# Kernel tuning notes

Measured on AMD Instinct MI355X. Metric: run time of the kernel, lower is better.

Reference implementation:

```python
import jax, jax.numpy as jnp
import numpy as np

THRESH = 0.3   # vis_threshold (score filter and final keep threshold)
SIGMA = 0.5    # Gaussian soft-NMS sigma (method=2 in classic soft_nms)
B, N = 16, 2048


def setup_inputs() -> dict:
    key = jax.random.key(0)
    k1, k2, k3 = jax.random.split(key, 3)
    xy = jax.random.uniform(k1, (B, N, 2), dtype=jnp.float32) * 1024.0
    wh = jax.random.uniform(k2, (B, N, 2), dtype=jnp.float32) * 256.0 + 1.0
    scores = jax.random.uniform(k3, (B, N, 1), dtype=jnp.float32)
    detections = jnp.concatenate([xy, xy + wh, scores], axis=-1)  # [B,N,5]
    return {"detections": detections}


def _pairwise_iou(b):
    # b: [N,4] as (x1,y1,x2,y2); classic soft-NMS uses +1 area convention
    x1, y1, x2, y2 = b[:, 0], b[:, 1], b[:, 2], b[:, 3]
    area = (x2 - x1 + 1.0) * (y2 - y1 + 1.0)
    xx1 = jnp.maximum(x1[:, None], x1[None, :])
    yy1 = jnp.maximum(y1[:, None], y1[None, :])
    xx2 = jnp.minimum(x2[:, None], x2[None, :])
    yy2 = jnp.minimum(y2[:, None], y2[None, :])
    w = jnp.clip(xx2 - xx1 + 1.0, 0.0)
    h = jnp.clip(yy2 - yy1 + 1.0, 0.0)
    inter = w * h
    return inter / (area[:, None] + area[None, :] - inter)  # [N,N]


def _soft_nms_single(boxes, scores):
    # boxes: [N,4], scores: [N]
    n = scores.shape[0]
    iou = _pairwise_iou(boxes)            # [N,N]
    valid = scores > THRESH               # score-threshold prefilter
    s0 = jnp.where(valid, scores, 0.0)

    def step(carry, _):
        s, active = carry
        i = jnp.argmax(jnp.where(active, s, -1.0))     # greedy pick of max live score
        si = jnp.where(active[i], s[i], -1.0)          # -1 sentinel once all boxes consumed
        w = jnp.exp(-(iou[i] * iou[i]) / SIGMA)        # Gaussian decay (method=2)
        active = active.at[i].set(False)
        s = jnp.where(active, s * w, s)                # decay remaining live scores
        return (s, active), (i, si)

    _, (idx, picked) = jax.lax.scan(step, (s0, valid), None, length=n)
    # score each box carried at the moment it was picked; .max ignores -1 sentinels
    final = jnp.full((n,), -1.0, scores.dtype).at[idx].max(picked)
    keep = final > THRESH
    return final, keep


def reference(detections):
    boxes = detections[..., :4]   # [B,N,4]
    scores = detections[..., 4]   # [B,N]
    final, keep = jax.vmap(_soft_nms_single)(boxes, scores)
    return final, keep
```

## Files before the change

kernel.cpp:

```cpp
#include <hip/hip_runtime.h>
#include <stdint.h>

static constexpr float kThresh = 0.3f;
static constexpr int N    = 2048;
static constexpr int NT   = 256;
static constexpr int LPT  = N / NT;
static constexpr int NW   = NT / 64;
static constexpr int KMAX = 8;

using u64 = unsigned long long;
using u32 = unsigned int;

template <int CTRL>
__device__ __forceinline__ u64 dpp_max_u64_step(u64 k) {
    const int lo  = (int)(u32)k;
    const int hi  = (int)(u32)(k >> 32);
    const int mlo = __builtin_amdgcn_update_dpp(lo, lo, CTRL, 0xF, 0xF, false);
    const int mhi = __builtin_amdgcn_update_dpp(hi, hi, CTRL, 0xF, 0xF, false);
    const u64 m   = ((u64)(u32)mhi << 32) | (u32)mlo;
    return (m > k) ? m : k;
}
__device__ __forceinline__ u64 wave_max_u64(u64 k) {
    k = dpp_max_u64_step<0x111>(k);
    k = dpp_max_u64_step<0x112>(k);
    k = dpp_max_u64_step<0x114>(k);
    k = dpp_max_u64_step<0x118>(k);
    k = dpp_max_u64_step<0x142>(k);
    k = dpp_max_u64_step<0x143>(k);
    const int lo = __builtin_amdgcn_readlane((int)(u32)k, 63);
    const int hi = __builtin_amdgcn_readlane((int)(u32)(k >> 32), 63);
    return ((u64)(u32)hi << 32) | (u32)lo;
}

struct Pick {
    u32    mid;
    float4 box;
    float  area;
};

template <int K>
__device__ __forceinline__ u64 decay_and_keys(
        float (&sr)[KMAX], const float (&x1)[KMAX], const float (&y1)[KMAX],
        const float (&x2)[KMAX], const float (&y2)[KMAX], const float (&ar)[KMAX],
        const u32 (&jp)[KMAX], const Pick& w)
{
    u64 kmax = 0ULL;
    #pragma unroll
    for (int e = 0; e < K; ++e) {
        if (jp[e] == w.mid) sr[e] = -1.0f;
        const float xx1 = fmaxf(w.box.x, x1[e]);
        const float yy1 = fmaxf(w.box.y, y1[e]);
        const float xx2 = fminf(w.box.z, x2[e]);
        const float yy2 = fminf(w.box.w, y2[e]);
        const float ww  = fmaxf(xx2 - xx1 + 1.0f, 0.0f);
        const float hh  = fmaxf(yy2 - yy1 + 1.0f, 0.0f);
        const float inter = ww * hh;
        const float iou   = inter / (w.area + ar[e] - inter);
        sr[e] *= expf(-(iou * iou) * 2.0f);
        const u64 key = ((u64)(__float_as_uint(sr[e]) + 1u) << 32) | jp[e];
        const u64 kk  = (sr[e] >= 0.0f) ? key : 0ULL;
        if (kk > kmax) kmax = kk;
    }
    return kmax;
}

template <int K>
__device__ __forceinline__ void fill_slots(
        float (&sr)[KMAX], float (&x1)[KMAX], float (&y1)[KMAX],
        float (&x2)[KMAX], float (&y2)[KMAX], float (&ar)[KMAX], u32 (&jp)[KMAX],
        const int* slist, const float* srs, const float4* sbox, const float* sarea,
        int t, int alive)
{
    #pragma unroll
    for (int e = 0; e < K; ++e) {
        const int pos = t + NT * e;
        if (pos < alive) {
            const int j = slist[pos];
            sr[e] = srs[pos];
            const float4 bb = sbox[j];
            x1[e] = bb.x; y1[e] = bb.y; x2[e] = bb.z; y2[e] = bb.w;
            ar[e] = sarea[j];
            jp[e] = ((u32)(N - 1 - j) << 21) | ((u32)t << 13) | ((u32)e << 10);
        } else {
            sr[e] = -1.0f;
            x1[e] = 3.0e38f; y1[e] = 3.0e38f; x2[e] = -3.0e38f; y2[e] = -3.0e38f;
            ar[e] = 1.0f;
            jp[e] = 0x3FFu;
        }
    }
}

template <int K>
__device__ __forceinline__ void run_tier(
        int& alive, int& k, Pick& w,
        float (&sr)[KMAX], float (&x1)[KMAX], float (&y1)[KMAX],
        float (&x2)[KMAX], float (&y2)[KMAX], float (&ar)[KMAX], u32 (&jp)[KMAX],
        int* slist, float* srs, const float4* sbox, const float* sarea, float* sfin,
        u64 (*redk)[NW], int* swave, int t, int lane, int wid)
{
    const int floorA = (K > 1) ? NT * (K - 1) : 0;
    if (alive <= floorA) return;

    fill_slots<K>(sr, x1, y1, x2, y2, ar, jp, slist, srs, sbox, sarea, t, alive);

    const int passes = alive - floorA;
    for (int p = 0; p < passes; ++p) {
        const u64 kmax = decay_and_keys<K>(sr, x1, y1, x2, y2, ar, jp, w);
        const u64 wmax = wave_max_u64(kmax);
        const bool writer = (wmax != 0ULL) ? (kmax == wmax) : (lane == 0);
        if (writer) redk[k & 1][wid] = wmax;
        __syncthreads();
        u64 best = redk[k & 1][0];
        #pragma unroll
        for (int q = 1; q < NW; ++q) {
            const u64 o = redk[k & 1][q];
            if (o > best) best = o;
        }
        const u32 lo   = (u32)best;
        const int winJ = (N - 1) - (int)(lo >> 21);
        w.mid = lo & 0xFFFFFC00u;
        if (t == 0) sfin[winJ] = __uint_as_float((u32)(best >> 32) - 1u);
        w.box  = sbox[winJ];
        w.area = sarea[winJ];
        ++k;
    }
    alive = floorA;

    if (K > 1) {
        (void)decay_and_keys<K>(sr, x1, y1, x2, y2, ar, jp, w);
        w.mid  = 0xFFFFFFFFu;
        w.box  = make_float4(3.0e38f, 3.0e38f, -3.0e38f, -3.0e38f);
        w.area = 1.0f;
        int c = 0;
        #pragma unroll
        for (int e = 0; e < K; ++e) c += (sr[e] >= 0.0f) ? 1 : 0;
        int pfx = c;
        #pragma unroll
        for (int d = 1; d < 64; d <<= 1) {
            const int v = __shfl_up(pfx, d, 64);
            if (lane >= d) pfx += v;
        }
        if (lane == 63) swave[wid] = pfx;
        __syncthreads();
        int wbase = 0;
        #pragma unroll
        for (int q = 0; q < NW; ++q)
            if (q < wid) wbase += swave[q];
        int mypos = wbase + (pfx - c);
        #pragma unroll
        for (int e = 0; e < K; ++e) {
            if (sr[e] >= 0.0f) {
                slist[mypos] = (N - 1) - (int)(jp[e] >> 21);
                srs[mypos]   = sr[e];
                ++mypos;
            }
        }
        __syncthreads();
    }
}

__launch_bounds__(NT, 1)
__global__ void soft_nms_kernel(const float* __restrict__ det,
                                float* __restrict__ out, int B)
{
    const int b = blockIdx.x, t = threadIdx.x, lane = t & 63, wid = t >> 6;

    __shared__ float4 sbox[N];
    __shared__ float  sarea[N];
    __shared__ float  sfin[N];
    __shared__ float  srs[N];
    __shared__ int    slist[N];
    __shared__ int    swave[NW];
    __shared__ u64    redk[2][NW];

    const float* dbase = det + (size_t)b * N * 5;

    float scv[LPT]; int lval = 0, c = 0;
    #pragma unroll
    for (int e = 0; e < LPT; ++e) {
        const int j = t * LPT + e;
        const float* p = dbase + (size_t)j * 5;
        const float X1 = p[0], Y1 = p[1], X2 = p[2], Y2 = p[3], SC = p[4];
        sbox[j]  = make_float4(X1, Y1, X2, Y2);
        sarea[j] = (X2 - X1 + 1.0f) * (Y2 - Y1 + 1.0f);
        sfin[j]  = -1.0f;
        scv[e]   = SC;
        const int va = SC > kThresh;
        lval |= va << e; c += va;
    }
    int pfx = c;
    #pragma unroll
    for (int d = 1; d < 64; d <<= 1) {
        const int v = __shfl_up(pfx, d, 64);
        if (lane >= d) pfx += v;
    }
    if (lane == 63) swave[wid] = pfx;
    __syncthreads();
    int wbase = 0, n0 = 0;
    #pragma unroll
    for (int q = 0; q < NW; ++q) {
        const int v = swave[q];
        if (q < wid) wbase += v;
        n0 += v;
    }
    int mypos = wbase + (pfx - c);
    #pragma unroll
    for (int e = 0; e < LPT; ++e)
        if ((lval >> e) & 1) { slist[mypos] = t * LPT + e; srs[mypos] = scv[e]; ++mypos; }
    __syncthreads();

    float sr[KMAX], x1[KMAX], y1[KMAX], x2[KMAX], y2[KMAX], ar[KMAX]; u32 jp[KMAX];
    int alive = n0, k = 0;
    Pick w;
    w.mid  = 0xFFFFFFFFu;
    w.box  = make_float4(3.0e38f, 3.0e38f, -3.0e38f, -3.0e38f);
    w.area = 1.0f;

    run_tier<8>(alive,k,w,sr,x1,y1,x2,y2,ar,jp,slist,srs,sbox,sarea,sfin,redk,swave,t,lane,wid);
    run_tier<7>(alive,k,w,sr,x1,y1,x2,y2,ar,jp,slist,srs,sbox,sarea,sfin,redk,swave,t,lane,wid);
    run_tier<6>(alive,k,w,sr,x1,y1,x2,y2,ar,jp,slist,srs,sbox,sarea,sfin,redk,swave,t,lane,wid);
    run_tier<5>(alive,k,w,sr,x1,y1,x2,y2,ar,jp,slist,srs,sbox,sarea,sfin,redk,swave,t,lane,wid);
    run_tier<4>(alive,k,w,sr,x1,y1,x2,y2,ar,jp,slist,srs,sbox,sarea,sfin,redk,swave,t,lane,wid);
    run_tier<3>(alive,k,w,sr,x1,y1,x2,y2,ar,jp,slist,srs,sbox,sarea,sfin,redk,swave,t,lane,wid);
    run_tier<2>(alive,k,w,sr,x1,y1,x2,y2,ar,jp,slist,srs,sbox,sarea,sfin,redk,swave,t,lane,wid);
    run_tier<1>(alive,k,w,sr,x1,y1,x2,y2,ar,jp,slist,srs,sbox,sarea,sfin,redk,swave,t,lane,wid);

    __syncthreads();
    float* of = out + (size_t)b * N;
    float* ok = out + (size_t)B * N + (size_t)b * N;
    #pragma unroll
    for (int e = 0; e < LPT; ++e) {
        const int j = t * LPT + e;
        const float f = sfin[j];
        of[j] = f;
        ok[j] = (f > kThresh) ? 1.0f : 0.0f;
    }
}

extern "C" void kernel_launch(void* const* d_in, const int* in_sizes, int n_in,
                              void* d_out, int out_size, void* d_ws, size_t ws_size,
                              hipStream_t stream) {
    const float* det = (const float*)d_in[0];
    float* out = (float*)d_out;
    const int B = in_sizes[0] / (N * 5);
    hipLaunchKernelGGL(soft_nms_kernel, dim3(B), dim3(NT), 0, stream, det, out, B);
}
```

Before: 1.000 ms.

## Pick two non-overlapping winners per soft-NMS step to halve serial iterations

Each step now finds the top two live scores (per-thread top-2, two wave reductions, cross-wave merge). If the two winning boxes do not intersect, their Gaussian decays commute, so both are committed in one iteration and their decays are applied together on the next pass. The goal is fewer serial block-wide barrier steps. Box areas are now recomputed from coordinates instead of read from a shared-memory array. In exchange, each pass does twice the IoU/exp work plus an extra wave reduction, and the speedup depends on how often the top two picks are disjoint.

```diff
diff --git a/kernel.cpp b/kernel.cpp
--- a/kernel.cpp
+++ b/kernel.cpp
@@ -32,44 +32,63 @@
     return ((u64)(u32)hi << 32) | (u32)lo;
 }
 
-struct Pick {
-    u32    mid;
-    float4 box;
-    float  area;
+struct Pick2 {
+    u32 mid1, mid2;
+    float4 b1, b2;
+    float a1, a2;
 };
+__device__ __forceinline__ void pick2_clear(Pick2& w) {
+    w.mid1 = 0xFFFFFFFFu; w.mid2 = 0xFFFFFFFFu;
+    w.b1 = make_float4(3.0e38f, 3.0e38f, -3.0e38f, -3.0e38f);
+    w.b2 = w.b1;
+    w.a1 = 1.0f; w.a2 = 1.0f;
+}
 
 template <int K>
-__device__ __forceinline__ u64 decay_and_keys(
+__device__ __forceinline__ void decay_and_keys2(
         float (&sr)[KMAX], const float (&x1)[KMAX], const float (&y1)[KMAX],
         const float (&x2)[KMAX], const float (&y2)[KMAX], const float (&ar)[KMAX],
-        const u32 (&jp)[KMAX], const Pick& w)
-{
-    u64 kmax = 0ULL;
+        const u32 (&jp)[KMAX], const Pick2& w, u64& k1o, u64& k2o)
+{
+    u64 k1 = 0ULL, k2 = 0ULL;
     #pragma unroll
     for (int e = 0; e < K; ++e) {
-        if (jp[e] == w.mid) sr[e] = -1.0f;
-        const float xx1 = fmaxf(w.box.x, x1[e]);
-        const float yy1 = fmaxf(w.box.y, y1[e]);
-        const float xx2 = fminf(w.box.z, x2[e]);
-        const float yy2 = fminf(w.box.w, y2[e]);
-        const float ww  = fmaxf(xx2 - xx1 + 1.0f, 0.0f);
-        const float hh  = fmaxf(yy2 - yy1 + 1.0f, 0.0f);
-        const float inter = ww * hh;
-        const float iou   = inter / (w.area + ar[e] - inter);
-        sr[e] *= expf(-(iou * iou) * 2.0f);
+        if (jp[e] == w.mid1 || jp[e] == w.mid2) sr[e] = -1.0f;
+        {
+            const float xx1 = fmaxf(w.b1.x, x1[e]);
+            const float yy1 = fmaxf(w.b1.y, y1[e]);
+            const float xx2 = fminf(w.b1.z, x2[e]);
+            const float yy2 = fminf(w.b1.w, y2[e]);
+            const float ww  = fmaxf(xx2 - xx1 + 1.0f, 0.0f);
+            const float hh  = fmaxf(yy2 - yy1 + 1.0f, 0.0f);
+            const float inter = ww * hh;
+            const float iou   = inter / (w.a1 + ar[e] - inter);
+            sr[e] *= expf(-(iou * iou) * 2.0f);
+        }
+        {
+            const float xx1 = fmaxf(w.b2.x, x1[e]);
+            const float yy1 = fmaxf(w.b2.y, y1[e]);
+            const float xx2 = fminf(w.b2.z, x2[e]);
+            const float yy2 = fminf(w.b2.w, y2[e]);
+            const float ww  = fmaxf(xx2 - xx1 + 1.0f, 0.0f);
+            const float hh  = fmaxf(yy2 - yy1 + 1.0f, 0.0f);
+            const float inter = ww * hh;
+            const float iou   = inter / (w.a2 + ar[e] - inter);
+            sr[e] *= expf(-(iou * iou) * 2.0f);
+        }
         const u64 key = ((u64)(__float_as_uint(sr[e]) + 1u) << 32) | jp[e];
-        const u64 kk  = (sr[e] >= 0.0f) ? key : 0ULL;
-        if (kk > kmax) kmax = kk;
-    }
-    return kmax;
+        const u64 kk  = (__float_as_int(sr[e]) >= 0) ? key : 0ULL;
+        if (kk > k1)      { k2 = k1; k1 = kk; }
+        else if (kk > k2) { k2 = kk; }
+    }
+    k1o = k1; k2o = k2;
 }
 
 template <int K>
 __device__ __forceinline__ void fill_slots(
         float (&sr)[KMAX], float (&x1)[KMAX], float (&y1)[KMAX],
         float (&x2)[KMAX], float (&y2)[KMAX], float (&ar)[KMAX], u32 (&jp)[KMAX],
-        const int* slist, const float* srs, const float4* sbox, const float* sarea,
-        int t, int alive)
+        const int* slist, const float* srs, const float4* sbox, int t, int alive)
 {
     #pragma unroll
     for (int e = 0; e < K; ++e) {
@@ -79,7 +98,7 @@
             sr[e] = srs[pos];
             const float4 bb = sbox[j];
             x1[e] = bb.x; y1[e] = bb.y; x2[e] = bb.z; y2[e] = bb.w;
-            ar[e] = sarea[j];
+            ar[e] = (bb.z - bb.x + 1.0f) * (bb.w - bb.y + 1.0f);
             jp[e] = ((u32)(N - 1 - j) << 21) | ((u32)t << 13) | ((u32)e << 10);
         } else {
             sr[e] = -1.0f;
@@ -92,48 +111,77 @@
 
 template <int K>
 __device__ __forceinline__ void run_tier(
-        int& alive, int& k, Pick& w,
+        int& alive, int& k, Pick2& w,
         float (&sr)[KMAX], float (&x1)[KMAX], float (&y1)[KMAX],
         float (&x2)[KMAX], float (&y2)[KMAX], float (&ar)[KMAX], u32 (&jp)[KMAX],
-        int* slist, float* srs, const float4* sbox, const float* sarea, float* sfin,
-        u64 (*redk)[NW], int* swave, int t, int lane, int wid)
+        int* slist, float* srs, const float4* sbox, float* sfin,
+        u64 (*redk)[NW][2], int* swave, int t, int lane, int wid)
 {
     const int floorA = (K > 1) ? NT * (K - 1) : 0;
     if (alive <= floorA) return;
 
-    fill_slots<K>(sr, x1, y1, x2, y2, ar, jp, slist, srs, sbox, sarea, t, alive);
-
-    const int passes = alive - floorA;
-    for (int p = 0; p < passes; ++p) {
-        const u64 kmax = decay_and_keys<K>(sr, x1, y1, x2, y2, ar, jp, w);
-        const u64 wmax = wave_max_u64(kmax);
-        const bool writer = (wmax != 0ULL) ? (kmax == wmax) : (lane == 0);
-        if (writer) redk[k & 1][wid] = wmax;
+    fill_slots<K>(sr, x1, y1, x2, y2, ar, jp, slist, srs, sbox, t, alive);
+
+    while (alive > floorA) {
+        const int par = k & 1;
+        u64 k1, k2;
+        decay_and_keys2<K>(sr, x1, y1, x2, y2, ar, jp, w, k1, k2);
+        const u64 wk1  = wave_max_u64(k1);
+        const u64 cand = (k1 == wk1) ? k2 : k1;
+        const u64 wk2  = wave_max_u64(cand);
+        if (lane == 0) { redk[par][wid][0] = wk1; redk[par][wid][1] = wk2; }
         __syncthreads();
-        u64 best = redk[k & 1][0];
-        #pragma unroll
-        for (int q = 1; q < NW; ++q) {
-            const u64 o = redk[k & 1][q];
-            if (o > best) best = o;
-        }
-        const u32 lo   = (u32)best;
-        const int winJ = (N - 1) - (int)(lo >> 21);
-        w.mid = lo & 0xFFFFFC00u;
-        if (t == 0) sfin[winJ] = __uint_as_float((u32)(best >> 32) - 1u);
-        w.box  = sbox[winJ];
-        w.area = sarea[winJ];
+
+        u64 r1[NW], r2[NW];
+        #pragma unroll
+        for (int q = 0; q < NW; ++q) { r1[q] = redk[par][q][0]; r2[q] = redk[par][q][1]; }
+        u64 gw1 = r1[0]; int ws = 0;
+        #pragma unroll
+        for (int q = 1; q < NW; ++q)
+            if (r1[q] > gw1) { gw1 = r1[q]; ws = q; }
+        u64 gw2 = 0ULL;
+        #pragma unroll
+        for (int q = 0; q < NW; ++q) {
+            const u64 c = (q == ws) ? r2[q] : r1[q];
+            if (c > gw2) gw2 = c;
+        }
+
+        const u32 lo1 = (u32)gw1;
+        const int j1  = (N - 1) - (int)(lo1 >> 21);
+        const u32 lo2 = (u32)gw2;
+        const int j2  = (gw2 != 0ULL) ? ((N - 1) - (int)(lo2 >> 21)) : 0;
+        const float4 b1 = sbox[j1];
+        const float4 b2 = sbox[j2];
+        const float a1 = (b1.z - b1.x + 1.0f) * (b1.w - b1.y + 1.0f);
+        const float a2 = (b2.z - b2.x + 1.0f) * (b2.w - b2.y + 1.0f);
+        const float cx1 = fmaxf(b1.x, b2.x), cy1 = fmaxf(b1.y, b2.y);
+        const float cx2 = fminf(b1.z, b2.z), cy2 = fminf(b1.w, b2.w);
+        const float cw  = fmaxf(cx2 - cx1 + 1.0f, 0.0f);
+        const float ch  = fmaxf(cy2 - cy1 + 1.0f, 0.0f);
+        const bool fast = (gw2 != 0ULL) && (cw * ch == 0.0f);
+
+        if (t == 0) {
+            sfin[j1] = __uint_as_float((u32)(gw1 >> 32) - 1u);
+            if (fast) sfin[j2] = __uint_as_float((u32)(gw2 >> 32) - 1u);
+        }
+        w.mid1 = lo1; w.b1 = b1; w.a1 = a1;
+        if (fast) { w.mid2 = lo2; w.b2 = b2; w.a2 = a2; }
+        else {
+            w.mid2 = 0xFFFFFFFFu;
+            w.b2 = make_float4(3.0e38f, 3.0e38f, -3.0e38f, -3.0e38f);
+            w.a2 = 1.0f;
+        }
+        alive -= fast ? 2 : 1;
         ++k;
     }
-    alive = floorA;
 
     if (K > 1) {
-        (void)decay_and_keys<K>(sr, x1, y1, x2, y2, ar, jp, w);
-        w.mid  = 0xFFFFFFFFu;
-        w.box  = make_float4(3.0e38f, 3.0e38f, -3.0e38f, -3.0e38f);
-        w.area = 1.0f;
+        u64 d1, d2;
+        decay_and_keys2<K>(sr, x1, y1, x2, y2, ar, jp, w, d1, d2);
+        pick2_clear(w);
         int c = 0;
         #pragma unroll
-        for (int e = 0; e < K; ++e) c += (sr[e] >= 0.0f) ? 1 : 0;
+        for (int e = 0; e < K; ++e) c += (__float_as_int(sr[e]) >= 0) ? 1 : 0;
         int pfx = c;
         #pragma unroll
         for (int d = 1; d < 64; d <<= 1) {
@@ -149,7 +197,7 @@
         int mypos = wbase + (pfx - c);
         #pragma unroll
         for (int e = 0; e < K; ++e) {
-            if (sr[e] >= 0.0f) {
+            if (__float_as_int(sr[e]) >= 0) {
                 slist[mypos] = (N - 1) - (int)(jp[e] >> 21);
                 srs[mypos]   = sr[e];
                 ++mypos;
@@ -166,12 +214,11 @@
     const int b = blockIdx.x, t = threadIdx.x, lane = t & 63, wid = t >> 6;
 
     __shared__ float4 sbox[N];
-    __shared__ float  sarea[N];
     __shared__ float  sfin[N];
     __shared__ float  srs[N];
     __shared__ int    slist[N];
     __shared__ int    swave[NW];
-    __shared__ u64    redk[2][NW];
+    __shared__ u64    redk[2][NW][2];
 
     const float* dbase = det + (size_t)b * N * 5;
 
@@ -181,10 +228,9 @@
         const int j = t * LPT + e;
         const float* p = dbase + (size_t)j * 5;
         const float X1 = p[0], Y1 = p[1], X2 = p[2], Y2 = p[3], SC = p[4];
-        sbox[j]  = make_float4(X1, Y1, X2, Y2);
-        sarea[j] = (X2 - X1 + 1.0f) * (Y2 - Y1 + 1.0f);
-        sfin[j]  = -1.0f;
-        scv[e]   = SC;
+        sbox[j] = make_float4(X1, Y1, X2, Y2);
+        sfin[j] = -1.0f;
+        scv[e]  = SC;
         const int va = SC > kThresh;
         lval |= va << e; c += va;
     }
@@ -211,19 +257,17 @@
 
     float sr[KMAX], x1[KMAX], y1[KMAX], x2[KMAX], y2[KMAX], ar[KMAX]; u32 jp[KMAX];
     int alive = n0, k = 0;
-    Pick w;
-    w.mid  = 0xFFFFFFFFu;
-    w.box  = make_float4(3.0e38f, 3.0e38f, -3.0e38f, -3.0e38f);
-    w.area = 1.0f;
-
-    run_tier<8>(alive,k,w,sr,x1,y1,x2,y2,ar,jp,slist,srs,sbox,sarea,sfin,redk,swave,t,lane,wid);
-    run_tier<7>(alive,k,w,sr,x1,y1,x2,y2,ar,jp,slist,srs,sbox,sarea,sfin,redk,swave,t,lane,wid);
-    run_tier<6>(alive,k,w,sr,x1,y1,x2,y2,ar,jp,slist,srs,sbox,sarea,sfin,redk,swave,t,lane,wid);
-    run_tier<5>(alive,k,w,sr,x1,y1,x2,y2,ar,jp,slist,srs,sbox,sarea,sfin,redk,swave,t,lane,wid);
-    run_tier<4>(alive,k,w,sr,x1,y1,x2,y2,ar,jp,slist,srs,sbox,sarea,sfin,redk,swave,t,lane,wid);
-    run_tier<3>(alive,k,w,sr,x1,y1,x2,y2,ar,jp,slist,srs,sbox,sarea,sfin,redk,swave,t,lane,wid);
-    run_tier<2>(alive,k,w,sr,x1,y1,x2,y2,ar,jp,slist,srs,sbox,sarea,sfin,redk,swave,t,lane,wid);
-    run_tier<1>(alive,k,w,sr,x1,y1,x2,y2,ar,jp,slist,srs,sbox,sarea,sfin,redk,swave,t,lane,wid);
+    Pick2 w;
+    pick2_clear(w);
+
+    run_tier<8>(alive,k,w,sr,x1,y1,x2,y2,ar,jp,slist,srs,sbox,sfin,redk,swave,t,lane,wid);
+    run_tier<7>(alive,k,w,sr,x1,y1,x2,y2,ar,jp,slist,srs,sbox,sfin,redk,swave,t,lane,wid);
+    run_tier<6>(alive,k,w,sr,x1,y1,x2,y2,ar,jp,slist,srs,sbox,sfin,redk,swave,t,lane,wid);
+    run_tier<5>(alive,k,w,sr,x1,y1,x2,y2,ar,jp,slist,srs,sbox,sfin,redk,swave,t,lane,wid);
+    run_tier<4>(alive,k,w,sr,x1,y1,x2,y2,ar,jp,slist,srs,sbox,sfin,redk,swave,t,lane,wid);
+    run_tier<3>(alive,k,w,sr,x1,y1,x2,y2,ar,jp,slist,srs,sbox,sfin,redk,swave,t,lane,wid);
+    run_tier<2>(alive,k,w,sr,x1,y1,x2,y2,ar,jp,slist,srs,sbox,sfin,redk,swave,t,lane,wid);
+    run_tier<1>(alive,k,w,sr,x1,y1,x2,y2,ar,jp,slist,srs,sbox,sfin,redk,swave,t,lane,wid);
 
     __syncthreads();
     float* of = out + (size_t)b * N;
```

Result: no change. 988.0 us (-1.2%).
